# Kernel tuning notes

Hardware: AMD Instinct MI355X
Metric: run time of the kernel (lower is better)

## Reference

```python
import jax, jax.numpy as jnp
import numpy as np
import math

N = 65536   # number of tree nodes
K = 4       # branching factor of the complete K-ary tree
D = 300     # input_size
H = 256     # hidden_size

def _levels(n, k):
    # complete k-ary tree: level l spans [start, start + k**l)
    levels, start, size = [], 0, 1
    while start < n:
        end = min(start + size, n)
        levels.append((start, end))
        start, size = end, size * k
    return levels

LEVELS = _levels(N, K)

def setup_inputs() -> dict:
    key = jax.random.key(0)
    ks = jax.random.split(key, 16)
    def U(k, shape, s):
        return jax.random.uniform(k, shape, jnp.float32, -s, s)
    s1 = 1.0 / math.sqrt(D + H)
    sfi = 1.0 / math.sqrt(D)
    sfh = 1.0 / math.sqrt(H)
    return {
        "inputs": jax.random.normal(ks[0], (N, D), jnp.float32),
        "ix_w": U(ks[1], (H, D), s1), "ix_b": U(ks[2], (H,), s1),
        "ih_w": U(ks[3], (H, H), s1), "ih_b": U(ks[4], (H,), s1),
        "ux_w": U(ks[5], (H, D), s1), "ux_b": U(ks[6], (H,), s1),
        "uh_w": U(ks[7], (H, H), s1), "uh_b": U(ks[8], (H,), s1),
        "fi_w": U(ks[9], (H, D), sfi), "fi_b": U(ks[10], (H,), sfi),
        "fh_w": U(ks[11], (H, H), sfh), "fh_b": U(ks[12], (H,), sfh),
    }

def reference(inputs, ix_w, ix_b, ih_w, ih_b, ux_w, ux_b, uh_w, uh_b,
              fi_w, fi_b, fh_w, fh_b):
    # Precompute all input projections once (batched over every node).
    ix = inputs @ ix_w.T + ix_b   # [N, H]
    ux = inputs @ ux_w.T + ux_b   # [N, H]
    fi = inputs @ fi_w.T + fi_b   # [N, H]
    h = jnp.zeros((N, H), inputs.dtype)
    c = jnp.zeros((N, H), inputs.dtype)
    # Bottom-up over tree levels (children before parents); level bounds static.
    for (s, e) in reversed(LEVELS):
        node = jnp.arange(s, e)                                   # [L]
        cidx = node[:, None] * K + 1 + jnp.arange(K)[None, :]     # [L, K]
        valid = cidx < N
        cidx = jnp.where(valid, cidx, 0)
        m = valid[..., None].astype(inputs.dtype)                 # [L, K, 1]
        hc = h[cidx] * m                                          # [L, K, H]
        cc = c[cidx] * m
        h_sum = hc.sum(axis=1)                                    # [L, H]
        # per-child forget gate: sigmoid(W_fi x + b_fi + W_fh h_k + b_fh)
        f = jax.nn.sigmoid(fi[s:e][:, None, :]
                           + jnp.einsum('lkh,gh->lkg', hc, fh_w) + fh_b)
        fc = (f * cc).sum(axis=1)                                 # masked via cc
        i = jax.nn.sigmoid(ix[s:e] + h_sum @ ih_w.T + ih_b)
        u = jnp.tanh(ux[s:e] + h_sum @ uh_w.T + uh_b)
        c_new = i * u + fc
        h_new = jnp.tanh(c_new)          # no output gate in this module
        h = h.at[s:e].set(h_new)
        c = c.at[s:e].set(c_new)
    # root node state (matches (next_h, [next_h, next_c]) at the root)
    return h[0], c[0]
```

## Files before the change

kernel.cpp:

```cpp
#include <hip/hip_runtime.h>
#include <hip/hip_bf16.h>


#define NTOT 65536
#define DD   300
#define KP   320
#define HH   256
#define LEAF_START 16384
#define LOG2E 1.4426950408889634f

typedef unsigned short u16;
typedef unsigned int   u32;
typedef __attribute__((ext_vector_type(8))) short bf16x8;
typedef __attribute__((ext_vector_type(4))) float f32x4;

#define OFF_HB    0ull
#define OFF_CB    33554944ull
#define OFF_PRE   67109888ull
#define OFF_WXB   92275712ull
#define OFF_WHB   92767232ull
#define OFF_XB    93160448ull
#define OFF_PIU   135103488ull
#define OFF_PF    146375680ull
#define OFF_HSB   168788992ull
#define OFF_BI    177243136ull
#define OFF_BU    177244160ull
#define OFF_BF    177245184ull

__device__ __forceinline__ float frcp(float x) { return __builtin_amdgcn_rcpf(x); }
__device__ __forceinline__ float fex2(float x) { return __builtin_amdgcn_exp2f(x); }
__device__ __forceinline__ float sigm(float x)  { return frcp(1.f + fex2(-LOG2E * x)); }
__device__ __forceinline__ float ftanh(float x) { return 1.f - 2.f * frcp(1.f + fex2(2.f * LOG2E * x)); }

__device__ __forceinline__ u16 f2bf(float f) {
    __hip_bfloat16 b = __float2bfloat16(f);
    u16 u; __builtin_memcpy(&u, &b, 2); return u;
}
__device__ __forceinline__ float bf2f(u16 b) {
    union { u32 u; float f; } v; v.u = ((u32)b) << 16;
    return v.f;
}
__device__ __forceinline__ int lidx(int r, int g) { return (r << 3) | (g ^ (r & 7)); }

__device__ __forceinline__ void gll16(const void* g, void* l) {
    __builtin_amdgcn_global_load_lds(
        (const __attribute__((address_space(1))) unsigned int*)g,
        (__attribute__((address_space(3))) unsigned int*)l, 16, 0, 0);
}

__global__ __launch_bounds__(256) void conv_all(
    const float* __restrict__ X,
    const float* __restrict__ ixw, const float* __restrict__ uxw,
    const float* __restrict__ fiw,
    const float* __restrict__ ihw, const float* __restrict__ uhw,
    const float* __restrict__ fhw,
    const float* __restrict__ ixb, const float* __restrict__ ihb,
    const float* __restrict__ uxb, const float* __restrict__ uhb,
    const float* __restrict__ fib, const float* __restrict__ fhb,
    u32* __restrict__ Xb2, u32* __restrict__ Wxb2, u32* __restrict__ Whb2,
    u16* __restrict__ hb, u16* __restrict__ cb,
    float* __restrict__ bI, float* __restrict__ bU, float* __restrict__ bF)
{
    const int b = blockIdx.x;
    const int t = threadIdx.x;
    if (b < 2048) {
        const size_t total = (size_t)NTOT * 160;
        for (size_t id = (size_t)b * 256 + t; id < total; id += (size_t)2048 * 256) {
            const int node = (int)(id / 160);
            const int k    = ((int)(id % 160)) * 2;
            const float f0 = (k < DD)     ? X[(size_t)node * DD + k]     : 0.f;
            const float f1 = (k + 1 < DD) ? X[(size_t)node * DD + k + 1] : 0.f;
            Xb2[id] = (u32)f2bf(f0) | ((u32)f2bf(f1) << 16);
        }
    } else if (b < 2528) {
        const int b2 = b - 2048;
        const int total = 768 * 160;
        for (int id = b2 * 256 + t; id < total; id += 480 * 256) {
            const int row = id / 160;
            const int k   = (id % 160) * 2;
            const float* src = (row < 256) ? (ixw + (size_t)row * DD)
                             : (row < 512) ? (uxw + (size_t)(row - 256) * DD)
                                           : (fiw + (size_t)(row - 512) * DD);
            const float f0 = (k < DD)     ? src[k]     : 0.f;
            const float f1 = (k + 1 < DD) ? src[k + 1] : 0.f;
            Wxb2[id] = (u32)f2bf(f0) | ((u32)f2bf(f1) << 16);
        }
    } else {
        const int b3 = b - 2528;
        if (b3 == 0) {
            hb[(size_t)NTOT * HH + t] = 0;
            cb[(size_t)NTOT * HH + t] = 0;
            bI[t] = ixb[t] + ihb[t];
            bU[t] = uxb[t] + uhb[t];
            bF[t] = fib[t] + fhb[t];
        }
        const int total = 768 * 128;
        for (int id = b3 * 256 + t; id < total; id += 384 * 256) {
            const int row = id / 128;
            const int k   = (id % 128) * 2;
            const float* src = (row < 256) ? (ihw + (size_t)row * HH)
                             : (row < 512) ? (uhw + (size_t)(row - 256) * HH)
                                           : (fhw + (size_t)(row - 512) * HH);
            Whb2[id] = (u32)f2bf(src[k]) | ((u32)f2bf(src[k + 1]) << 16);
        }
    }
}

__global__ __launch_bounds__(256) void leaf_gemm(
    const u16* __restrict__ Xb, const u16* __restrict__ Wxb,
    const float* __restrict__ bI, const float* __restrict__ bU,
    u16* __restrict__ hb, u16* __restrict__ cb)
{
    __shared__ bf16x8 Ash[2048];
    __shared__ bf16x8 Bsh[2048];

    const int tid  = threadIdx.x;
    const int lane = tid & 63;
    const int w    = tid >> 6;
    const int wr   = w >> 1, wc = w & 1;
    const int m16  = lane & 15, q = lane >> 4;

    const int row0   = LEAF_START + blockIdx.x * 128;
    const int chbase = blockIdx.y * 64;

    const bf16x8* __restrict__ Xv = (const bf16x8*)Xb;
    const bf16x8* __restrict__ Wv = (const bf16x8*)Wxb;

    auto stage = [&](int kt, int buf) {
        const int base = buf << 10;
        #pragma unroll
        for (int i = 0; i < 4; ++i) {
            const int sI = w * 256 + i * 64 + lane;
            const int r = sI >> 3, gs = sI & 7;
            const int g = gs ^ (r & 7);
            gll16(Xv + (size_t)(row0 + r) * 40 + kt * 8 + g, &Ash[base + sI]);
        }
        #pragma unroll
        for (int i = 0; i < 4; ++i) {
            const int sI = w * 256 + i * 64 + lane;
            const int br = sI >> 3, gs = sI & 7;
            const int g = gs ^ (br & 7);
            const int srow = ((br >> 6) << 8) + chbase + (br & 63);
            gll16(Wv + (size_t)srow * 40 + kt * 8 + g, &Bsh[base + sI]);
        }
    };

    f32x4 accI[4][2], accU[4][2];
    #pragma unroll
    for (int mf = 0; mf < 4; ++mf)
        #pragma unroll
        for (int nf = 0; nf < 2; ++nf) { accI[mf][nf] = (f32x4)0.f; accU[mf][nf] = (f32x4)0.f; }

    stage(0, 0);
    __syncthreads();
    for (int kt = 0; kt < 5; ++kt) {
        const int cur = kt & 1;
        if (kt < 4) stage(kt + 1, cur ^ 1);
        const int base = cur << 10;
        #pragma unroll
        for (int ks = 0; ks < 2; ++ks) {
            const int kg = ks * 4 + q;
            bf16x8 a[4], bIv[2], bUv[2];
            #pragma unroll
            for (int mf = 0; mf < 4; ++mf)
                a[mf] = Ash[base + lidx(wr * 64 + mf * 16 + m16, kg)];
            #pragma unroll
            for (int nf = 0; nf < 2; ++nf) {
                bIv[nf] = Bsh[base + lidx(wc * 32 + nf * 16 + m16, kg)];
                bUv[nf] = Bsh[base + lidx(64 + wc * 32 + nf * 16 + m16, kg)];
            }
            #pragma unroll
            for (int mf = 0; mf < 4; ++mf)
                #pragma unroll
                for (int nf = 0; nf < 2; ++nf) {
                    accI[mf][nf] = __builtin_amdgcn_mfma_f32_16x16x32_bf16(
                        a[mf], bIv[nf], accI[mf][nf], 0, 0, 0);
                    accU[mf][nf] = __builtin_amdgcn_mfma_f32_16x16x32_bf16(
                        a[mf], bUv[nf], accU[mf][nf], 0, 0, 0);
                }
        }
        __syncthreads();
    }

    #pragma unroll
    for (int nf = 0; nf < 2; ++nf) {
        const int ch = chbase + wc * 32 + nf * 16 + m16;
        const float bi = bI[ch];
        const float bu = bU[ch];
        #pragma unroll
        for (int mf = 0; mf < 4; ++mf) {
            #pragma unroll
            for (int r4 = 0; r4 < 4; ++r4) {
                const float cn = sigm(accI[mf][nf][r4] + bi) * ftanh(accU[mf][nf][r4] + bu);
                const int node = row0 + wr * 64 + mf * 16 + q * 4 + r4;
                const size_t off = (size_t)node * HH + ch;
                cb[off] = f2bf(cn);
                hb[off] = f2bf(ftanh(cn));
            }
        }
    }
}

__global__ __launch_bounds__(256) void proj_gemm(const u16* __restrict__ Xb,
                                                 const u16* __restrict__ Wxb,
                                                 u16* __restrict__ pre)
{
    __shared__ bf16x8 Ash[2048];
    __shared__ bf16x8 Bsh[2048];

    const int tid  = threadIdx.x;
    const int lane = tid & 63;
    const int w    = tid >> 6;
    const int wr   = w >> 1, wc = w & 1;
    const int m16  = lane & 15, q = lane >> 4;

    const int row0 = blockIdx.x * 128;
    const int n0   = blockIdx.y * 128;

    const bf16x8* __restrict__ Xv = (const bf16x8*)Xb;
    const bf16x8* __restrict__ Wv = (const bf16x8*)Wxb;

    auto stage = [&](int kt, int buf) {
        const int base = buf << 10;
        #pragma unroll
        for (int i = 0; i < 4; ++i) {
            const int sI = w * 256 + i * 64 + lane;
            const int r = sI >> 3, gs = sI & 7;
            const int g = gs ^ (r & 7);
            gll16(Xv + (size_t)(row0 + r) * 40 + kt * 8 + g, &Ash[base + sI]);
        }
        #pragma unroll
        for (int i = 0; i < 4; ++i) {
            const int sI = w * 256 + i * 64 + lane;
            const int br = sI >> 3, gs = sI & 7;
            const int g = gs ^ (br & 7);
            gll16(Wv + (size_t)(n0 + br) * 40 + kt * 8 + g, &Bsh[base + sI]);
        }
    };

    f32x4 acc[4][4];
    #pragma unroll
    for (int mf = 0; mf < 4; ++mf)
        #pragma unroll
        for (int nf = 0; nf < 4; ++nf) acc[mf][nf] = (f32x4)0.f;

    stage(0, 0);
    __syncthreads();
    for (int kt = 0; kt < 5; ++kt) {
        const int cur = kt & 1;
        if (kt < 4) stage(kt + 1, cur ^ 1);
        const int base = cur << 10;
        #pragma unroll
        for (int ks = 0; ks < 2; ++ks) {
            const int kg = ks * 4 + q;
            bf16x8 a[4], b[4];
            #pragma unroll
            for (int mf = 0; mf < 4; ++mf)
                a[mf] = Ash[base + lidx(wr * 64 + mf * 16 + m16, kg)];
            #pragma unroll
            for (int nf = 0; nf < 4; ++nf)
                b[nf] = Bsh[base + lidx(wc * 64 + nf * 16 + m16, kg)];
            #pragma unroll
            for (int mf = 0; mf < 4; ++mf)
                #pragma unroll
                for (int nf = 0; nf < 4; ++nf)
                    acc[mf][nf] = __builtin_amdgcn_mfma_f32_16x16x32_bf16(
                        a[mf], b[nf], acc[mf][nf], 0, 0, 0);
        }
        __syncthreads();
    }

    #pragma unroll
    for (int mf = 0; mf < 4; ++mf)
        #pragma unroll
        for (int nf = 0; nf < 4; ++nf) {
            const int col = n0 + wc * 64 + nf * 16 + m16;
            #pragma unroll
            for (int r4 = 0; r4 < 4; ++r4) {
                const int node = row0 + wr * 64 + mf * 16 + q * 4 + r4;
                pre[(size_t)node * 768 + col] = f2bf(acc[mf][nf][r4]);
            }
        }
}

__global__ __launch_bounds__(256) void hsum_big(const u32* __restrict__ hb2,
                                                u32* __restrict__ hsumb2)
{
    const int id = blockIdx.x * 256 + threadIdx.x;
    const int total = 12288 * 128;
    if (id >= total) return;
    const int ploc = id >> 7, j2 = id & 127;
    const int p = 4096 + ploc;
    const int c0 = 4 * p + 1;
    float s0 = 0.f, s1 = 0.f;
    #pragma unroll
    for (int k = 0; k < 4; ++k) {
        const u32 v = hb2[(size_t)(c0 + k) * 128 + j2];
        s0 += bf2f((u16)v);
        s1 += bf2f((u16)(v >> 16));
    }
    hsumb2[(size_t)p * 128 + j2] = (u32)f2bf(s0) | ((u32)f2bf(s1) << 16);
}

__global__ __launch_bounds__(256) void rec_gemm(const u16* __restrict__ hb,
                                                const u16* __restrict__ hsumb,
                                                const u16* __restrict__ Whb,
                                                u16* __restrict__ projIU,
                                                u16* __restrict__ projF,
                                                int crow0, int prow0, int L)
{
    __shared__ bf16x8 Ash[2048];
    __shared__ bf16x8 Bsh[2048];

    const int nIUrb = (L + 127) >> 7;
    const int bid   = blockIdx.x;

    bool isIU; int rb, cbk;
    if (bid < nIUrb * 4) { isIU = true;  rb = bid >> 2; cbk = bid & 3; }
    else { isIU = false; const int b2 = bid - nIUrb * 4; rb = b2 >> 1; cbk = b2 & 1; }

    const int row0  = rb * 128;
    const int Brow0 = isIU ? cbk * 128 : 512 + cbk * 128;
    const int ocol0 = cbk * 128;
    u16* __restrict__ out = isIU ? projIU : projF;
    const int ostride = isIU ? 512 : 256;

    const int tid  = threadIdx.x;
    const int lane = tid & 63;
    const int w    = tid >> 6;
    const int wr   = w >> 1, wc = w & 1;
    const int m16  = lane & 15, q = lane >> 4;

    const bf16x8* __restrict__ Av = isIU ? (const bf16x8*)hsumb : (const bf16x8*)hb;
    const bf16x8* __restrict__ Wv = (const bf16x8*)Whb;

    auto stage = [&](int kt, int buf) {
        const int base = buf << 10;
        #pragma unroll
        for (int i = 0; i < 4; ++i) {
            const int sI = w * 256 + i * 64 + lane;
            const int r = sI >> 3, gs = sI & 7;
            const int g = gs ^ (r & 7);
            int arow;
            if (isIU) arow = prow0 + row0 + r;
            else { arow = crow0 + row0 + r; if (arow > NTOT) arow = NTOT; }
            gll16(Av + (size_t)arow * 32 + kt * 8 + g, &Ash[base + sI]);
        }
        #pragma unroll
        for (int i = 0; i < 4; ++i) {
            const int sI = w * 256 + i * 64 + lane;
            const int br = sI >> 3, gs = sI & 7;
            const int g = gs ^ (br & 7);
            gll16(Wv + (size_t)(Brow0 + br) * 32 + kt * 8 + g, &Bsh[base + sI]);
        }
    };

    f32x4 acc[4][4];
    #pragma unroll
    for (int mf = 0; mf < 4; ++mf)
        #pragma unroll
        for (int nf = 0; nf < 4; ++nf) acc[mf][nf] = (f32x4)0.f;

    stage(0, 0);
    __syncthreads();
    for (int kt = 0; kt < 4; ++kt) {
        const int cur = kt & 1;
        if (kt < 3) stage(kt + 1, cur ^ 1);
        const int base = cur << 10;
        #pragma unroll
        for (int ks = 0; ks < 2; ++ks) {
            const int kg = ks * 4 + q;
            bf16x8 a[4], b[4];
            #pragma unroll
            for (int mf = 0; mf < 4; ++mf)
                a[mf] = Ash[base + lidx(wr * 64 + mf * 16 + m16, kg)];
            #pragma unroll
            for (int nf = 0; nf < 4; ++nf)
                b[nf] = Bsh[base + lidx(wc * 64 + nf * 16 + m16, kg)];
            #pragma unroll
            for (int mf = 0; mf < 4; ++mf)
                #pragma unroll
                for (int nf = 0; nf < 4; ++nf)
                    acc[mf][nf] = __builtin_amdgcn_mfma_f32_16x16x32_bf16(
                        a[mf], b[nf], acc[mf][nf], 0, 0, 0);
        }
        __syncthreads();
    }

    #pragma unroll
    for (int mf = 0; mf < 4; ++mf)
        #pragma unroll
        for (int nf = 0; nf < 4; ++nf) {
            const int col = ocol0 + wc * 64 + nf * 16 + m16;
            #pragma unroll
            for (int r4 = 0; r4 < 4; ++r4) {
                const int orow = row0 + wr * 64 + mf * 16 + q * 4 + r4;
                out[(size_t)orow * ostride + col] = f2bf(acc[mf][nf][r4]);
            }
        }
}

__global__ __launch_bounds__(256) void gate_kernel(
    const u32* __restrict__ pre2, const u32* __restrict__ pIU2,
    const u32* __restrict__ pF2,
    const float* __restrict__ bI, const float* __restrict__ bU,
    const float* __restrict__ bF,
    u32* __restrict__ hb2, u32* __restrict__ cb2, u32* __restrict__ hsumb2,
    float* __restrict__ out, int s, int crow0, int L)
{
    const int t  = threadIdx.x;
    const int j2 = t & 127;
    const float2 vbi = ((const float2*)bI)[j2];
    const float2 vbu = ((const float2*)bU)[j2];
    const float2 vbf = ((const float2*)bF)[j2];

    if (L == 1) {
        if (t >= 128) return;
        const u32 pi = pre2[j2];
        const u32 pu = pre2[128 + j2];
        const u32 pf = pre2[256 + j2];
        const u32 ri = pIU2[j2];
        const u32 ru = pIU2[128 + j2];
        const float aI0 = bf2f((u16)pi) + bf2f((u16)ri) + vbi.x;
        const float aI1 = bf2f((u16)(pi >> 16)) + bf2f((u16)(ri >> 16)) + vbi.y;
        const float aU0 = bf2f((u16)pu) + bf2f((u16)ru) + vbu.x;
        const float aU1 = bf2f((u16)(pu >> 16)) + bf2f((u16)(ru >> 16)) + vbu.y;
        const float fp0 = bf2f((u16)pf) + vbf.x;
        const float fp1 = bf2f((u16)(pf >> 16)) + vbf.y;
        float fc0 = 0.f, fc1 = 0.f;
        #pragma unroll
        for (int kk = 0; kk < 4; ++kk) {
            const u32 rf = pF2[(size_t)kk * 128 + j2];
            const u32 cc = cb2[(size_t)(crow0 + kk) * 128 + j2];
            fc0 = fmaf(sigm(fp0 + bf2f((u16)rf)), bf2f((u16)cc), fc0);
            fc1 = fmaf(sigm(fp1 + bf2f((u16)(rf >> 16))), bf2f((u16)(cc >> 16)), fc1);
        }
        const float cn0 = fmaf(sigm(aI0), ftanh(aU0), fc0);
        const float cn1 = fmaf(sigm(aI1), ftanh(aU1), fc1);
        const float hn0 = ftanh(cn0);
        const float hn1 = ftanh(cn1);
        hb2[j2] = (u32)f2bf(hn0) | ((u32)f2bf(hn1) << 16);
        cb2[j2] = (u32)f2bf(cn0) | ((u32)f2bf(cn1) << 16);
        ((float2*)out)[j2] = make_float2(hn0, hn1);
        ((float2*)(out + 256))[j2] = make_float2(cn0, cn1);
        return;
    }

    const int ng = (L + 3) >> 2;
    const int g  = blockIdx.x * 2 + (t >> 7);
    if (g >= ng) return;
    const int p = ((s - 1) >> 2) + g;

    float hs0 = 0.f, hs1 = 0.f;
    #pragma unroll
    for (int k = 0; k < 4; ++k) {
        const int nloc = 4 * g + k;
        const int n = s + nloc;
        if (nloc < L) {
            const u32 pi = pre2[(size_t)n * 384 + j2];
            const u32 pu = pre2[(size_t)n * 384 + 128 + j2];
            const u32 pf = pre2[(size_t)n * 384 + 256 + j2];
            const u32 ri = pIU2[(size_t)nloc * 256 + j2];
            const u32 ru = pIU2[(size_t)nloc * 256 + 128 + j2];
            const float aI0 = bf2f((u16)pi) + bf2f((u16)ri) + vbi.x;
            const float aI1 = bf2f((u16)(pi >> 16)) + bf2f((u16)(ri >> 16)) + vbi.y;
            const float aU0 = bf2f((u16)pu) + bf2f((u16)ru) + vbu.x;
            const float aU1 = bf2f((u16)(pu >> 16)) + bf2f((u16)(ru >> 16)) + vbu.y;
            const float fp0 = bf2f((u16)pf) + vbf.x;
            const float fp1 = bf2f((u16)(pf >> 16)) + vbf.y;
            float fc0 = 0.f, fc1 = 0.f;
            #pragma unroll
            for (int kk = 0; kk < 4; ++kk) {
                const u32 rf = pF2[(size_t)(4 * nloc + kk) * 128 + j2];
                const u32 cc = cb2[(size_t)(crow0 + 4 * nloc + kk) * 128 + j2];
                fc0 = fmaf(sigm(fp0 + bf2f((u16)rf)), bf2f((u16)cc), fc0);
                fc1 = fmaf(sigm(fp1 + bf2f((u16)(rf >> 16))), bf2f((u16)(cc >> 16)), fc1);
            }
            const float cn0 = fmaf(sigm(aI0), ftanh(aU0), fc0);
            const float cn1 = fmaf(sigm(aI1), ftanh(aU1), fc1);
            const float hn0 = ftanh(cn0);
            const float hn1 = ftanh(cn1);
            hb2[(size_t)n * 128 + j2] = (u32)f2bf(hn0) | ((u32)f2bf(hn1) << 16);
            cb2[(size_t)n * 128 + j2] = (u32)f2bf(cn0) | ((u32)f2bf(cn1) << 16);
            hs0 += hn0; hs1 += hn1;
        } else {
            const u32 v = hb2[(size_t)n * 128 + j2];
            hs0 += bf2f((u16)v);
            hs1 += bf2f((u16)(v >> 16));
        }
    }
    hsumb2[(size_t)p * 128 + j2] = (u32)f2bf(hs0) | ((u32)f2bf(hs1) << 16);
}

extern "C" void kernel_launch(void* const* d_in, const int* in_sizes, int n_in,
                              void* d_out, int out_size, void* d_ws, size_t ws_size,
                              hipStream_t stream) {
    const float* X   = (const float*)d_in[0];
    const float* ixw = (const float*)d_in[1];
    const float* ixb = (const float*)d_in[2];
    const float* ihw = (const float*)d_in[3];
    const float* ihb = (const float*)d_in[4];
    const float* uxw = (const float*)d_in[5];
    const float* uxb = (const float*)d_in[6];
    const float* uhw = (const float*)d_in[7];
    const float* uhb = (const float*)d_in[8];
    const float* fiw = (const float*)d_in[9];
    const float* fib = (const float*)d_in[10];
    const float* fhw = (const float*)d_in[11];
    const float* fhb = (const float*)d_in[12];
    float* out = (float*)d_out;

    char* ws = (char*)d_ws;
    u16* hb   = (u16*)(ws + OFF_HB);
    u16* cb   = (u16*)(ws + OFF_CB);
    u16* pre  = (u16*)(ws + OFF_PRE);
    u16* Wxb  = (u16*)(ws + OFF_WXB);
    u16* Whb  = (u16*)(ws + OFF_WHB);
    u16* Xb   = (u16*)(ws + OFF_XB);
    u16* pIU  = (u16*)(ws + OFF_PIU);
    u16* pF   = (u16*)(ws + OFF_PF);
    u16* hsb  = (u16*)(ws + OFF_HSB);
    float* bI = (float*)(ws + OFF_BI);
    float* bU = (float*)(ws + OFF_BU);
    float* bF = (float*)(ws + OFF_BF);

    conv_all<<<2912, 256, 0, stream>>>(X, ixw, uxw, fiw, ihw, uhw, fhw,
        ixb, ihb, uxb, uhb, fib, fhb,
        (u32*)Xb, (u32*)Wxb, (u32*)Whb, hb, cb, bI, bU, bF);

    leaf_gemm<<<dim3(384, 4), 256, 0, stream>>>(Xb, Wxb, bI, bU, hb, cb);
    proj_gemm<<<dim3(128, 6), 256, 0, stream>>>(Xb, Wxb, pre);
    hsum_big<<<6144, 256, 0, stream>>>((const u32*)hb, (u32*)hsb);

    const int starts[8] = {5461, 1365, 341, 85, 21, 5, 1, 0};
    const int ends[8]   = {16384, 5461, 1365, 341, 85, 21, 5, 1};
    for (int l = 0; l < 8; ++l) {
        const int s = starts[l], e = ends[l];
        const int L = e - s;
        const int crow0 = 4 * s + 1;
        const int nIUrb = (L + 127) >> 7;
        const int nFrb  = (4 * L + 127) >> 7;
        rec_gemm<<<nIUrb * 4 + nFrb * 2, 256, 0, stream>>>(hb, hsb, Whb, pIU, pF,
                                                           crow0, s, L);
        const int ng = (L + 3) >> 2;
        gate_kernel<<<(ng + 1) >> 1, 256, 0, stream>>>(
            (const u32*)pre, (const u32*)pIU, (const u32*)pF, bI, bU, bF,
            (u32*)hb, (u32*)cb, (u32*)hsb, out, s, crow0, L);
    }
}
```

Measured before the change: 198.8 us.

## Fuse leaf/proj GEMMs, compute child h-sum in rec_gemm, move forget-gate reduction into epilogue

The separate leaf and input-projection GEMM launches are merged into one grid with branch-by-block-index, and the standalone hsum_big kernel is removed. For the first internal level, rec_gemm now sums the four children's h on the fly while staging the A tile, and the remaining level-5 h-sums are computed by extra blocks appended to the gate kernel. The forget-gate sigmoid and child-cell reduction move into the rec_gemm epilogue, which writes an fp32 fc buffer instead of a bf16 projected-F buffer. This cuts kernel launches and intermediate traffic, in exchange for more work and scattered cb/pre reads in the GEMM epilogue.

Measured after the change: 198.3 us. About the same (-0.3%).

```diff
diff --git a/kernel.cpp b/kernel.cpp
--- a/kernel.cpp
+++ b/kernel.cpp
@@ -13,6 +13,8 @@
 typedef unsigned int   u32;
 typedef __attribute__((ext_vector_type(8))) short bf16x8;
 typedef __attribute__((ext_vector_type(4))) float f32x4;
+
+union BF8 { bf16x8 v; u16 u[8]; };
 
 #define OFF_HB    0ull
 #define OFF_CB    33554944ull
@@ -21,11 +23,11 @@
 #define OFF_WHB   92767232ull
 #define OFF_XB    93160448ull
 #define OFF_PIU   135103488ull
-#define OFF_PF    146375680ull
-#define OFF_HSB   168788992ull
-#define OFF_BI    177243136ull
-#define OFF_BU    177244160ull
-#define OFF_BF    177245184ull
+#define OFF_FC    146375680ull
+#define OFF_HSB   157647872ull
+#define OFF_BI    166102016ull
+#define OFF_BU    166103040ull
+#define OFF_BF    166104064ull
 
 __device__ __forceinline__ float frcp(float x) { return __builtin_amdgcn_rcpf(x); }
 __device__ __forceinline__ float fex2(float x) { return __builtin_amdgcn_exp2f(x); }
@@ -106,10 +108,10 @@
     }
 }
 
-__global__ __launch_bounds__(256) void leaf_gemm(
+__global__ __launch_bounds__(256) void lp_gemm(
     const u16* __restrict__ Xb, const u16* __restrict__ Wxb,
     const float* __restrict__ bI, const float* __restrict__ bU,
-    u16* __restrict__ hb, u16* __restrict__ cb)
+    u16* __restrict__ hb, u16* __restrict__ cb, u16* __restrict__ pre)
 {
     __shared__ bf16x8 Ash[2048];
     __shared__ bf16x8 Bsh[2048];
@@ -120,93 +122,175 @@
     const int wr   = w >> 1, wc = w & 1;
     const int m16  = lane & 15, q = lane >> 4;
 
-    const int row0   = LEAF_START + blockIdx.x * 128;
-    const int chbase = blockIdx.y * 64;
-
     const bf16x8* __restrict__ Xv = (const bf16x8*)Xb;
     const bf16x8* __restrict__ Wv = (const bf16x8*)Wxb;
 
-    auto stage = [&](int kt, int buf) {
-        const int base = buf << 10;
-        #pragma unroll
-        for (int i = 0; i < 4; ++i) {
-            const int sI = w * 256 + i * 64 + lane;
-            const int r = sI >> 3, gs = sI & 7;
-            const int g = gs ^ (r & 7);
-            gll16(Xv + (size_t)(row0 + r) * 40 + kt * 8 + g, &Ash[base + sI]);
-        }
-        #pragma unroll
-        for (int i = 0; i < 4; ++i) {
-            const int sI = w * 256 + i * 64 + lane;
-            const int br = sI >> 3, gs = sI & 7;
-            const int g = gs ^ (br & 7);
-            const int srow = ((br >> 6) << 8) + chbase + (br & 63);
-            gll16(Wv + (size_t)srow * 40 + kt * 8 + g, &Bsh[base + sI]);
-        }
-    };
-
-    f32x4 accI[4][2], accU[4][2];
-    #pragma unroll
-    for (int mf = 0; mf < 4; ++mf)
-        #pragma unroll
-        for (int nf = 0; nf < 2; ++nf) { accI[mf][nf] = (f32x4)0.f; accU[mf][nf] = (f32x4)0.f; }
-
-    stage(0, 0);
-    __syncthreads();
-    for (int kt = 0; kt < 5; ++kt) {
-        const int cur = kt & 1;
-        if (kt < 4) stage(kt + 1, cur ^ 1);
-        const int base = cur << 10;
-        #pragma unroll
-        for (int ks = 0; ks < 2; ++ks) {
-            const int kg = ks * 4 + q;
-            bf16x8 a[4], bIv[2], bUv[2];
-            #pragma unroll
-            for (int mf = 0; mf < 4; ++mf)
-                a[mf] = Ash[base + lidx(wr * 64 + mf * 16 + m16, kg)];
-            #pragma unroll
-            for (int nf = 0; nf < 2; ++nf) {
-                bIv[nf] = Bsh[base + lidx(wc * 32 + nf * 16 + m16, kg)];
-                bUv[nf] = Bsh[base + lidx(64 + wc * 32 + nf * 16 + m16, kg)];
-            }
-            #pragma unroll
-            for (int mf = 0; mf < 4; ++mf)
+    if (blockIdx.x < 1536) {
+        const int row0   = LEAF_START + (blockIdx.x >> 2) * 128;
+        const int chbase = (blockIdx.x & 3) * 64;
+
+        auto stage = [&](int kt, int buf) {
+            const int base = buf << 10;
+            #pragma unroll
+            for (int i = 0; i < 4; ++i) {
+                const int sI = w * 256 + i * 64 + lane;
+                const int r = sI >> 3, gs = sI & 7;
+                const int g = gs ^ (r & 7);
+                gll16(Xv + (size_t)(row0 + r) * 40 + kt * 8 + g, &Ash[base + sI]);
+            }
+            #pragma unroll
+            for (int i = 0; i < 4; ++i) {
+                const int sI = w * 256 + i * 64 + lane;
+                const int br = sI >> 3, gs = sI & 7;
+                const int g = gs ^ (br & 7);
+                const int srow = ((br >> 6) << 8) + chbase + (br & 63);
+                gll16(Wv + (size_t)srow * 40 + kt * 8 + g, &Bsh[base + sI]);
+            }
+        };
+
+        f32x4 accI[4][2], accU[4][2];
+        #pragma unroll
+        for (int mf = 0; mf < 4; ++mf)
+            #pragma unroll
+            for (int nf = 0; nf < 2; ++nf) { accI[mf][nf] = (f32x4)0.f; accU[mf][nf] = (f32x4)0.f; }
+
+        stage(0, 0);
+        __syncthreads();
+        for (int kt = 0; kt < 5; ++kt) {
+            const int cur = kt & 1;
+            if (kt < 4) stage(kt + 1, cur ^ 1);
+            const int base = cur << 10;
+            #pragma unroll
+            for (int ks = 0; ks < 2; ++ks) {
+                const int kg = ks * 4 + q;
+                bf16x8 a[4], bIv[2], bUv[2];
+                #pragma unroll
+                for (int mf = 0; mf < 4; ++mf)
+                    a[mf] = Ash[base + lidx(wr * 64 + mf * 16 + m16, kg)];
                 #pragma unroll
                 for (int nf = 0; nf < 2; ++nf) {
-                    accI[mf][nf] = __builtin_amdgcn_mfma_f32_16x16x32_bf16(
-                        a[mf], bIv[nf], accI[mf][nf], 0, 0, 0);
-                    accU[mf][nf] = __builtin_amdgcn_mfma_f32_16x16x32_bf16(
-                        a[mf], bUv[nf], accU[mf][nf], 0, 0, 0);
-                }
-        }
+                    bIv[nf] = Bsh[base + lidx(wc * 32 + nf * 16 + m16, kg)];
+                    bUv[nf] = Bsh[base + lidx(64 + wc * 32 + nf * 16 + m16, kg)];
+                }
+                #pragma unroll
+                for (int mf = 0; mf < 4; ++mf)
+                    #pragma unroll
+                    for (int nf = 0; nf < 2; ++nf) {
+                        accI[mf][nf] = __builtin_amdgcn_mfma_f32_16x16x32_bf16(
+                            a[mf], bIv[nf], accI[mf][nf], 0, 0, 0);
+                        accU[mf][nf] = __builtin_amdgcn_mfma_f32_16x16x32_bf16(
+                            a[mf], bUv[nf], accU[mf][nf], 0, 0, 0);
+                    }
+            }
+            __syncthreads();
+        }
+
+        #pragma unroll
+        for (int nf = 0; nf < 2; ++nf) {
+            const int ch = chbase + wc * 32 + nf * 16 + m16;
+            const float bi = bI[ch];
+            const float bu = bU[ch];
+            #pragma unroll
+            for (int mf = 0; mf < 4; ++mf) {
+                #pragma unroll
+                for (int r4 = 0; r4 < 4; ++r4) {
+                    const float cn = sigm(accI[mf][nf][r4] + bi) * ftanh(accU[mf][nf][r4] + bu);
+                    const int node = row0 + wr * 64 + mf * 16 + q * 4 + r4;
+                    const size_t off = (size_t)node * HH + ch;
+                    cb[off] = f2bf(cn);
+                    hb[off] = f2bf(ftanh(cn));
+                }
+            }
+        }
+    } else {
+        const int pb   = blockIdx.x - 1536;
+        const int row0 = (pb / 6) * 128;
+        const int n0   = (pb % 6) * 128;
+
+        auto stage = [&](int kt, int buf) {
+            const int base = buf << 10;
+            #pragma unroll
+            for (int i = 0; i < 4; ++i) {
+                const int sI = w * 256 + i * 64 + lane;
+                const int r = sI >> 3, gs = sI & 7;
+                const int g = gs ^ (r & 7);
+                gll16(Xv + (size_t)(row0 + r) * 40 + kt * 8 + g, &Ash[base + sI]);
+            }
+            #pragma unroll
+            for (int i = 0; i < 4; ++i) {
+                const int sI = w * 256 + i * 64 + lane;
+                const int br = sI >> 3, gs = sI & 7;
+                const int g = gs ^ (br & 7);
+                gll16(Wv + (size_t)(n0 + br) * 40 + kt * 8 + g, &Bsh[base + sI]);
+            }
+        };
+
+        f32x4 acc[4][4];
+        #pragma unroll
+        for (int mf = 0; mf < 4; ++mf)
+            #pragma unroll
+            for (int nf = 0; nf < 4; ++nf) acc[mf][nf] = (f32x4)0.f;
+
+        stage(0, 0);
         __syncthreads();
-    }
-
-    #pragma unroll
-    for (int nf = 0; nf < 2; ++nf) {
-        const int ch = chbase + wc * 32 + nf * 16 + m16;
-        const float bi = bI[ch];
-        const float bu = bU[ch];
-        #pragma unroll
-        for (int mf = 0; mf < 4; ++mf) {
-            #pragma unroll
-            for (int r4 = 0; r4 < 4; ++r4) {
-                const float cn = sigm(accI[mf][nf][r4] + bi) * ftanh(accU[mf][nf][r4] + bu);
-                const int node = row0 + wr * 64 + mf * 16 + q * 4 + r4;
-                const size_t off = (size_t)node * HH + ch;
-                cb[off] = f2bf(cn);
-                hb[off] = f2bf(ftanh(cn));
-            }
-        }
-    }
-}
-
-__global__ __launch_bounds__(256) void proj_gemm(const u16* __restrict__ Xb,
-                                                 const u16* __restrict__ Wxb,
-                                                 u16* __restrict__ pre)
+        for (int kt = 0; kt < 5; ++kt) {
+            const int cur = kt & 1;
+            if (kt < 4) stage(kt + 1, cur ^ 1);
+            const int base = cur << 10;
+            #pragma unroll
+            for (int ks = 0; ks < 2; ++ks) {
+                const int kg = ks * 4 + q;
+                bf16x8 a[4], b[4];
+                #pragma unroll
+                for (int mf = 0; mf < 4; ++mf)
+                    a[mf] = Ash[base + lidx(wr * 64 + mf * 16 + m16, kg)];
+                #pragma unroll
+                for (int nf = 0; nf < 4; ++nf)
+                    b[nf] = Bsh[base + lidx(wc * 64 + nf * 16 + m16, kg)];
+                #pragma unroll
+                for (int mf = 0; mf < 4; ++mf)
+                    #pragma unroll
+                    for (int nf = 0; nf < 4; ++nf)
+                        acc[mf][nf] = __builtin_amdgcn_mfma_f32_16x16x32_bf16(
+                            a[mf], b[nf], acc[mf][nf], 0, 0, 0);
+            }
+            __syncthreads();
+        }
+
+        #pragma unroll
+        for (int mf = 0; mf < 4; ++mf)
+            #pragma unroll
+            for (int nf = 0; nf < 4; ++nf) {
+                const int col = n0 + wc * 64 + nf * 16 + m16;
+                #pragma unroll
+                for (int r4 = 0; r4 < 4; ++r4) {
+                    const int node = row0 + wr * 64 + mf * 16 + q * 4 + r4;
+                    pre[(size_t)node * 768 + col] = f2bf(acc[mf][nf][r4]);
+                }
+            }
+    }
+}
+
+__global__ __launch_bounds__(256) void rec_gemm(
+    const u16* __restrict__ hb, const u16* __restrict__ hsb,
+    const u16* __restrict__ Whb, const u16* __restrict__ pre,
+    const float* __restrict__ bF, const u16* __restrict__ cb,
+    u16* __restrict__ projIU, float* __restrict__ fcbuf,
+    int s, int crow0, int L, int bigIU)
 {
     __shared__ bf16x8 Ash[2048];
     __shared__ bf16x8 Bsh[2048];
+
+    const int nIUrb = (L + 127) >> 7;
+    const int bid   = blockIdx.x;
+
+    bool isIU; int rb, cbk;
+    if (bid < nIUrb * 4) { isIU = true;  rb = bid >> 2; cbk = bid & 3; }
+    else { isIU = false; const int b2 = bid - nIUrb * 4; rb = b2 >> 1; cbk = b2 & 1; }
+
+    const int row0  = rb * 128;
+    const int Brow0 = isIU ? cbk * 128 : 512 + cbk * 128;
+    const int ocol0 = cbk * 128;
 
     const int tid  = threadIdx.x;
     const int lane = tid & 63;
@@ -214,137 +298,50 @@
     const int wr   = w >> 1, wc = w & 1;
     const int m16  = lane & 15, q = lane >> 4;
 
-    const int row0 = blockIdx.x * 128;
-    const int n0   = blockIdx.y * 128;
-
-    const bf16x8* __restrict__ Xv = (const bf16x8*)Xb;
-    const bf16x8* __restrict__ Wv = (const bf16x8*)Wxb;
+    const bf16x8* __restrict__ Hv = (const bf16x8*)hb;
+    const bf16x8* __restrict__ Sv = (const bf16x8*)hsb;
+    const bf16x8* __restrict__ Wv = (const bf16x8*)Whb;
 
     auto stage = [&](int kt, int buf) {
         const int base = buf << 10;
-        #pragma unroll
-        for (int i = 0; i < 4; ++i) {
-            const int sI = w * 256 + i * 64 + lane;
-            const int r = sI >> 3, gs = sI & 7;
-            const int g = gs ^ (r & 7);
-            gll16(Xv + (size_t)(row0 + r) * 40 + kt * 8 + g, &Ash[base + sI]);
-        }
-        #pragma unroll
-        for (int i = 0; i < 4; ++i) {
-            const int sI = w * 256 + i * 64 + lane;
-            const int br = sI >> 3, gs = sI & 7;
-            const int g = gs ^ (br & 7);
-            gll16(Wv + (size_t)(n0 + br) * 40 + kt * 8 + g, &Bsh[base + sI]);
-        }
-    };
-
-    f32x4 acc[4][4];
-    #pragma unroll
-    for (int mf = 0; mf < 4; ++mf)
-        #pragma unroll
-        for (int nf = 0; nf < 4; ++nf) acc[mf][nf] = (f32x4)0.f;
-
-    stage(0, 0);
-    __syncthreads();
-    for (int kt = 0; kt < 5; ++kt) {
-        const int cur = kt & 1;
-        if (kt < 4) stage(kt + 1, cur ^ 1);
-        const int base = cur << 10;
-        #pragma unroll
-        for (int ks = 0; ks < 2; ++ks) {
-            const int kg = ks * 4 + q;
-            bf16x8 a[4], b[4];
-            #pragma unroll
-            for (int mf = 0; mf < 4; ++mf)
-                a[mf] = Ash[base + lidx(wr * 64 + mf * 16 + m16, kg)];
-            #pragma unroll
-            for (int nf = 0; nf < 4; ++nf)
-                b[nf] = Bsh[base + lidx(wc * 64 + nf * 16 + m16, kg)];
-            #pragma unroll
-            for (int mf = 0; mf < 4; ++mf)
-                #pragma unroll
-                for (int nf = 0; nf < 4; ++nf)
-                    acc[mf][nf] = __builtin_amdgcn_mfma_f32_16x16x32_bf16(
-                        a[mf], b[nf], acc[mf][nf], 0, 0, 0);
-        }
-        __syncthreads();
-    }
-
-    #pragma unroll
-    for (int mf = 0; mf < 4; ++mf)
-        #pragma unroll
-        for (int nf = 0; nf < 4; ++nf) {
-            const int col = n0 + wc * 64 + nf * 16 + m16;
-            #pragma unroll
-            for (int r4 = 0; r4 < 4; ++r4) {
-                const int node = row0 + wr * 64 + mf * 16 + q * 4 + r4;
-                pre[(size_t)node * 768 + col] = f2bf(acc[mf][nf][r4]);
-            }
-        }
-}
-
-__global__ __launch_bounds__(256) void hsum_big(const u32* __restrict__ hb2,
-                                                u32* __restrict__ hsumb2)
-{
-    const int id = blockIdx.x * 256 + threadIdx.x;
-    const int total = 12288 * 128;
-    if (id >= total) return;
-    const int ploc = id >> 7, j2 = id & 127;
-    const int p = 4096 + ploc;
-    const int c0 = 4 * p + 1;
-    float s0 = 0.f, s1 = 0.f;
-    #pragma unroll
-    for (int k = 0; k < 4; ++k) {
-        const u32 v = hb2[(size_t)(c0 + k) * 128 + j2];
-        s0 += bf2f((u16)v);
-        s1 += bf2f((u16)(v >> 16));
-    }
-    hsumb2[(size_t)p * 128 + j2] = (u32)f2bf(s0) | ((u32)f2bf(s1) << 16);
-}
-
-__global__ __launch_bounds__(256) void rec_gemm(const u16* __restrict__ hb,
-                                                const u16* __restrict__ hsumb,
-                                                const u16* __restrict__ Whb,
-                                                u16* __restrict__ projIU,
-                                                u16* __restrict__ projF,
-                                                int crow0, int prow0, int L)
-{
-    __shared__ bf16x8 Ash[2048];
-    __shared__ bf16x8 Bsh[2048];
-
-    const int nIUrb = (L + 127) >> 7;
-    const int bid   = blockIdx.x;
-
-    bool isIU; int rb, cbk;
-    if (bid < nIUrb * 4) { isIU = true;  rb = bid >> 2; cbk = bid & 3; }
-    else { isIU = false; const int b2 = bid - nIUrb * 4; rb = b2 >> 1; cbk = b2 & 1; }
-
-    const int row0  = rb * 128;
-    const int Brow0 = isIU ? cbk * 128 : 512 + cbk * 128;
-    const int ocol0 = cbk * 128;
-    u16* __restrict__ out = isIU ? projIU : projF;
-    const int ostride = isIU ? 512 : 256;
-
-    const int tid  = threadIdx.x;
-    const int lane = tid & 63;
-    const int w    = tid >> 6;
-    const int wr   = w >> 1, wc = w & 1;
-    const int m16  = lane & 15, q = lane >> 4;
-
-    const bf16x8* __restrict__ Av = isIU ? (const bf16x8*)hsumb : (const bf16x8*)hb;
-    const bf16x8* __restrict__ Wv = (const bf16x8*)Whb;
-
-    auto stage = [&](int kt, int buf) {
-        const int base = buf << 10;
-        #pragma unroll
-        for (int i = 0; i < 4; ++i) {
-            const int sI = w * 256 + i * 64 + lane;
-            const int r = sI >> 3, gs = sI & 7;
-            const int g = gs ^ (r & 7);
-            int arow;
-            if (isIU) arow = prow0 + row0 + r;
-            else { arow = crow0 + row0 + r; if (arow > NTOT) arow = NTOT; }
-            gll16(Av + (size_t)arow * 32 + kt * 8 + g, &Ash[base + sI]);
+        if (isIU && bigIU) {
+            #pragma unroll
+            for (int i = 0; i < 4; ++i) {
+                const int G = tid + i * 256;
+                const int r = G >> 3, g = G & 7;
+                bf16x8 val;
+                if (row0 + r < L) {
+                    const size_t cg0 = (size_t)(crow0 + 4 * (row0 + r)) * 32 + kt * 8 + g;
+                    BF8 x0, x1, x2, x3, o;
+                    x0.v = Hv[cg0]; x1.v = Hv[cg0 + 32];
+                    x2.v = Hv[cg0 + 64]; x3.v = Hv[cg0 + 96];
+                    #pragma unroll
+                    for (int j = 0; j < 8; ++j)
+                        o.u[j] = f2bf(bf2f(x0.u[j]) + bf2f(x1.u[j])
+                                    + bf2f(x2.u[j]) + bf2f(x3.u[j]));
+                    val = o.v;
+                } else {
+                    BF8 z;
+                    #pragma unroll
+                    for (int j = 0; j < 8; ++j) z.u[j] = 0;
+                    val = z.v;
+                }
+                Ash[base + lidx(r, g)] = val;
+            }
+        } else {
+            #pragma unroll
+            for (int i = 0; i < 4; ++i) {
+                const int sI = w * 256 + i * 64 + lane;
+                const int r = sI >> 3, gs = sI & 7;
+                const int g = gs ^ (r & 7);
+                if (isIU) {
+                    gll16(Sv + (size_t)(s + row0 + r) * 32 + kt * 8 + g, &Ash[base + sI]);
+                } else {
+                    int arow = crow0 + row0 + r;
+                    if (arow > NTOT) arow = NTOT;
+                    gll16(Hv + (size_t)arow * 32 + kt * 8 + g, &Ash[base + sI]);
+                }
+            }
         }
         #pragma unroll
         for (int i = 0; i < 4; ++i) {
@@ -387,56 +384,68 @@
         __syncthreads();
     }
 
-    #pragma unroll
-    for (int mf = 0; mf < 4; ++mf)
-        #pragma unroll
-        for (int nf = 0; nf < 4; ++nf) {
-            const int col = ocol0 + wc * 64 + nf * 16 + m16;
-            #pragma unroll
-            for (int r4 = 0; r4 < 4; ++r4) {
-                const int orow = row0 + wr * 64 + mf * 16 + q * 4 + r4;
-                out[(size_t)orow * ostride + col] = f2bf(acc[mf][nf][r4]);
-            }
-        }
+    if (isIU) {
+        #pragma unroll
+        for (int mf = 0; mf < 4; ++mf)
+            #pragma unroll
+            for (int nf = 0; nf < 4; ++nf) {
+                const int col = ocol0 + wc * 64 + nf * 16 + m16;
+                #pragma unroll
+                for (int r4 = 0; r4 < 4; ++r4) {
+                    const int orow = row0 + wr * 64 + mf * 16 + q * 4 + r4;
+                    projIU[(size_t)orow * 512 + col] = f2bf(acc[mf][nf][r4]);
+                }
+            }
+    } else {
+        #pragma unroll
+        for (int mf = 0; mf < 4; ++mf) {
+            const int off  = wr * 64 + mf * 16 + q * 4;
+            const int goff = (row0 + off) >> 2;
+            if (goff < L) {
+                #pragma unroll
+                for (int nf = 0; nf < 4; ++nf) {
+                    const int col = ocol0 + wc * 64 + nf * 16 + m16;
+                    const float fpre = bf2f(pre[(size_t)(s + goff) * 768 + 512 + col]) + bF[col];
+                    float fc = 0.f;
+                    #pragma unroll
+                    for (int r4 = 0; r4 < 4; ++r4) {
+                        int child = crow0 + row0 + off + r4;
+                        if (child > NTOT) child = NTOT;
+                        const float cc = bf2f(cb[(size_t)child * HH + col]);
+                        fc = fmaf(sigm(acc[mf][nf][r4] + fpre), cc, fc);
+                    }
+                    fcbuf[(size_t)goff * HH + col] = fc;
+                }
+            }
+        }
+    }
 }
 
 __global__ __launch_bounds__(256) void gate_kernel(
     const u32* __restrict__ pre2, const u32* __restrict__ pIU2,
-    const u32* __restrict__ pF2,
+    const float* __restrict__ fcbuf,
     const float* __restrict__ bI, const float* __restrict__ bU,
-    const float* __restrict__ bF,
     u32* __restrict__ hb2, u32* __restrict__ cb2, u32* __restrict__ hsumb2,
-    float* __restrict__ out, int s, int crow0, int L)
+    float* __restrict__ out, int s, int L)
 {
     const int t  = threadIdx.x;
     const int j2 = t & 127;
-    const float2 vbi = ((const float2*)bI)[j2];
-    const float2 vbu = ((const float2*)bU)[j2];
-    const float2 vbf = ((const float2*)bF)[j2];
 
     if (L == 1) {
         if (t >= 128) return;
+        const float2 vbi = ((const float2*)bI)[j2];
+        const float2 vbu = ((const float2*)bU)[j2];
         const u32 pi = pre2[j2];
         const u32 pu = pre2[128 + j2];
-        const u32 pf = pre2[256 + j2];
         const u32 ri = pIU2[j2];
         const u32 ru = pIU2[128 + j2];
         const float aI0 = bf2f((u16)pi) + bf2f((u16)ri) + vbi.x;
         const float aI1 = bf2f((u16)(pi >> 16)) + bf2f((u16)(ri >> 16)) + vbi.y;
         const float aU0 = bf2f((u16)pu) + bf2f((u16)ru) + vbu.x;
         const float aU1 = bf2f((u16)(pu >> 16)) + bf2f((u16)(ru >> 16)) + vbu.y;
-        const float fp0 = bf2f((u16)pf) + vbf.x;
-        const float fp1 = bf2f((u16)(pf >> 16)) + vbf.y;
-        float fc0 = 0.f, fc1 = 0.f;
-        #pragma unroll
-        for (int kk = 0; kk < 4; ++kk) {
-            const u32 rf = pF2[(size_t)kk * 128 + j2];
-            const u32 cc = cb2[(size_t)(crow0 + kk) * 128 + j2];
-            fc0 = fmaf(sigm(fp0 + bf2f((u16)rf)), bf2f((u16)cc), fc0);
-            fc1 = fmaf(sigm(fp1 + bf2f((u16)(rf >> 16))), bf2f((u16)(cc >> 16)), fc1);
-        }
-        const float cn0 = fmaf(sigm(aI0), ftanh(aU0), fc0);
-        const float cn1 = fmaf(sigm(aI1), ftanh(aU1), fc1);
+        const float2 fc = ((const float2*)fcbuf)[j2];
+        const float cn0 = fmaf(sigm(aI0), ftanh(aU0), fc.x);
+        const float cn1 = fmaf(sigm(aI1), ftanh(aU1), fc.y);
         const float hn0 = ftanh(cn0);
         const float hn1 = ftanh(cn1);
         hb2[j2] = (u32)f2bf(hn0) | ((u32)f2bf(hn1) << 16);
@@ -447,7 +456,28 @@
     }
 
     const int ng = (L + 3) >> 2;
-    const int g  = blockIdx.x * 2 + (t >> 7);
+    const int gateBlocks = (ng + 1) >> 1;
+    if ((int)blockIdx.x >= gateBlocks) {
+        const int id = ((int)blockIdx.x - gateBlocks) * 256 + t;
+        if (id < 1365 * 128) {
+            const int ploc = id >> 7, jj = id & 127;
+            const int p = 4096 + ploc;
+            const int c0 = 4 * p + 1;
+            float s0 = 0.f, s1 = 0.f;
+            #pragma unroll
+            for (int k = 0; k < 4; ++k) {
+                const u32 v = hb2[(size_t)(c0 + k) * 128 + jj];
+                s0 += bf2f((u16)v);
+                s1 += bf2f((u16)(v >> 16));
+            }
+            hsumb2[(size_t)p * 128 + jj] = (u32)f2bf(s0) | ((u32)f2bf(s1) << 16);
+        }
+        return;
+    }
+
+    const float2 vbi = ((const float2*)bI)[j2];
+    const float2 vbu = ((const float2*)bU)[j2];
+    const int g = blockIdx.x * 2 + (t >> 7);
     if (g >= ng) return;
     const int p = ((s - 1) >> 2) + g;
 
@@ -459,25 +489,15 @@
         if (nloc < L) {
             const u32 pi = pre2[(size_t)n * 384 + j2];
             const u32 pu = pre2[(size_t)n * 384 + 128 + j2];
-            const u32 pf = pre2[(size_t)n * 384 + 256 + j2];
             const u32 ri = pIU2[(size_t)nloc * 256 + j2];
             const u32 ru = pIU2[(size_t)nloc * 256 + 128 + j2];
             const float aI0 = bf2f((u16)pi) + bf2f((u16)ri) + vbi.x;
             const float aI1 = bf2f((u16)(pi >> 16)) + bf2f((u16)(ri >> 16)) + vbi.y;
             const float aU0 = bf2f((u16)pu) + bf2f((u16)ru) + vbu.x;
             const float aU1 = bf2f((u16)(pu >> 16)) + bf2f((u16)(ru >> 16)) + vbu.y;
-            const float fp0 = bf2f((u16)pf) + vbf.x;
-            const float fp1 = bf2f((u16)(pf >> 16)) + vbf.y;
-            float fc0 = 0.f, fc1 = 0.f;
-            #pragma unroll
-            for (int kk = 0; kk < 4; ++kk) {
-                const u32 rf = pF2[(size_t)(4 * nloc + kk) * 128 + j2];
-                const u32 cc = cb2[(size_t)(crow0 + 4 * nloc + kk) * 128 + j2];
-                fc0 = fmaf(sigm(fp0 + bf2f((u16)rf)), bf2f((u16)cc), fc0);
-                fc1 = fmaf(sigm(fp1 + bf2f((u16)(rf >> 16))), bf2f((u16)(cc >> 16)), fc1);
-            }
-            const float cn0 = fmaf(sigm(aI0), ftanh(aU0), fc0);
-            const float cn1 = fmaf(sigm(aI1), ftanh(aU1), fc1);
+            const float2 fc = ((const float2*)fcbuf)[(size_t)nloc * 128 + j2];
+            const float cn0 = fmaf(sigm(aI0), ftanh(aU0), fc.x);
+            const float cn1 = fmaf(sigm(aI1), ftanh(aU1), fc.y);
             const float hn0 = ftanh(cn0);
             const float hn1 = ftanh(cn1);
             hb2[(size_t)n * 128 + j2] = (u32)f2bf(hn0) | ((u32)f2bf(hn1) << 16);
@@ -518,7 +538,7 @@
     u16* Whb  = (u16*)(ws + OFF_WHB);
     u16* Xb   = (u16*)(ws + OFF_XB);
     u16* pIU  = (u16*)(ws + OFF_PIU);
-    u16* pF   = (u16*)(ws + OFF_PF);
+    float* fc = (float*)(ws + OFF_FC);
     u16* hsb  = (u16*)(ws + OFF_HSB);
     float* bI = (float*)(ws + OFF_BI);
     float* bU = (float*)(ws + OFF_BU);
@@ -528,9 +548,7 @@
         ixb, ihb, uxb, uhb, fib, fhb,
         (u32*)Xb, (u32*)Wxb, (u32*)Whb, hb, cb, bI, bU, bF);
 
-    leaf_gemm<<<dim3(384, 4), 256, 0, stream>>>(Xb, Wxb, bI, bU, hb, cb);
-    proj_gemm<<<dim3(128, 6), 256, 0, stream>>>(Xb, Wxb, pre);
-    hsum_big<<<6144, 256, 0, stream>>>((const u32*)hb, (u32*)hsb);
+    lp_gemm<<<2304, 256, 0, stream>>>(Xb, Wxb, bI, bU, hb, cb, pre);
 
     const int starts[8] = {5461, 1365, 341, 85, 21, 5, 1, 0};
     const int ends[8]   = {16384, 5461, 1365, 341, 85, 21, 5, 1};
@@ -540,11 +558,13 @@
         const int crow0 = 4 * s + 1;
         const int nIUrb = (L + 127) >> 7;
         const int nFrb  = (4 * L + 127) >> 7;
-        rec_gemm<<<nIUrb * 4 + nFrb * 2, 256, 0, stream>>>(hb, hsb, Whb, pIU, pF,
-                                                           crow0, s, L);
+        rec_gemm<<<nIUrb * 4 + nFrb * 2, 256, 0, stream>>>(hb, hsb, Whb, pre, bF, cb,
+            pIU, fc, s, crow0, L, (l == 0) ? 1 : 0);
         const int ng = (L + 3) >> 2;
-        gate_kernel<<<(ng + 1) >> 1, 256, 0, stream>>>(
-            (const u32*)pre, (const u32*)pIU, (const u32*)pF, bI, bU, bF,
-            (u32*)hb, (u32*)cb, (u32*)hsb, out, s, crow0, L);
-    }
-}
+        const int gateBlocks = (ng + 1) >> 1;
+        const int hsBlocks = (l == 0) ? 683 : 0;
+        gate_kernel<<<gateBlocks + hsBlocks, 256, 0, stream>>>(
+            (const u32*)pre, (const u32*)pIU, fc, bI, bU,
+            (u32*)hb, (u32*)cb, (u32*)hsb, out, s, L);
+    }
+}
```
